# Kernel tuning notes

Hardware: AMD Instinct MI355X
Metric: run time of the kernel (lower is better)

## Reference

```python
import jax, jax.numpy as jnp
import numpy as np

NUM_INPUTS = 16
NUM_HIDDEN = 256
NUM_LAYERS = 4
B = 16384


def setup_inputs() -> dict:
    key = jax.random.key(0)
    ks = jax.random.split(key, 8)
    H, N, L = NUM_HIDDEN, NUM_INPUTS, NUM_LAYERS
    x0 = jax.random.normal(ks[0], (B, N), dtype=jnp.float32)
    # input layer: Linear(2 -> H)
    W_in = jax.random.normal(ks[1], (2, H), dtype=jnp.float32) * (1.0 / np.sqrt(2.0))
    b_in = jnp.zeros((H,), dtype=jnp.float32)
    # L-1 intermediate layers: Linear(2H -> H), stacked
    W_mid = jax.random.normal(ks[2], (L - 1, 2 * H, H), dtype=jnp.float32) * (1.0 / np.sqrt(2.0 * H))
    b_mid = jnp.zeros((L - 1, H), dtype=jnp.float32)
    # slater: Linear(H -> N) with xavier-normal weight, zero bias
    W_sl = jax.random.normal(ks[3], (H, N), dtype=jnp.float32) * np.sqrt(2.0 / (H + N))
    b_sl = jnp.zeros((N,), dtype=jnp.float32)
    width = jnp.full((1,), 0.1, dtype=jnp.float32)
    return {"x0": x0, "W_in": W_in, "b_in": b_in, "W_mid": W_mid,
            "b_mid": b_mid, "W_sl": W_sl, "b_sl": b_sl, "width": width}


def _forward(x0, W_in, b_in, W_mid, b_mid, W_sl, b_sl, width):
    N = x0.shape[1]
    # input equivariant layer: f = stack(h, mean(h)) -> [B, N, 2]
    g = jnp.broadcast_to(x0.mean(axis=1, keepdims=True), x0.shape)
    f = jnp.stack((x0, g), axis=2)                       # [B, N, 2]
    h = jnp.tanh(jnp.einsum('bnf,fh->bnh', f, W_in) + b_in)  # [B, N, H]
    # intermediate equivariant layers with residual
    for i in range(W_mid.shape[0]):
        gm = jnp.broadcast_to(h.mean(axis=1, keepdims=True), h.shape)
        fm = jnp.concatenate((h, gm), axis=2)            # [B, N, 2H]
        h = jnp.tanh(jnp.einsum('bnf,fh->bnh', fm, W_mid[i]) + b_mid[i]) + h
    # slog slater determinant
    slater = jnp.einsum('bnh,hm->bnm', h, W_sl) + b_sl   # [B, N, N]
    sign, logabsdet = jnp.linalg.slogdet(slater)
    log_factorial = jnp.log(jnp.arange(1, N + 1, dtype=jnp.float32)).sum()
    log_bcs = -width[0] * jnp.sum(x0 ** 2, axis=1)       # [B]
    return sign, logabsdet - 0.5 * log_factorial + log_bcs


def reference(x0, W_in, b_in, W_mid, b_mid, W_sl, b_sl, width):
    return _forward(x0, W_in, b_in, W_mid, b_mid, W_sl, b_sl, width)
```

## Files before the change

kernel.cpp:

```cpp
#include <hip/hip_runtime.h>

#define BTOT 16384
#define NI   16
#define HD   256
#define BB   4
#define NMID 3
#define ASH  264
#define SLS  20
#define HALF_LOGFACT 15.3359295387f

typedef short  bf16x8 __attribute__((ext_vector_type(8)));
typedef float  f32x4  __attribute__((ext_vector_type(4)));

__device__ __forceinline__ unsigned short f2bf(float f) {
    unsigned u = __builtin_bit_cast(unsigned, f);
    u += 0x7FFFu + ((u >> 16) & 1u);
    return (unsigned short)(u >> 16);
}
__device__ __forceinline__ unsigned cvt_pk_bf16(float lo, float hi) {
    unsigned d;
    asm("v_cvt_pk_bf16_f32 %0, %1, %2" : "=v"(d) : "v"(lo), "v"(hi));
    return d;
}
__device__ __forceinline__ float bflo(unsigned u) { return __builtin_bit_cast(float, u << 16); }
__device__ __forceinline__ float bfhi(unsigned u) { return __builtin_bit_cast(float, u & 0xFFFF0000u); }
__device__ __forceinline__ float bcast(float x, int lane) {
    return __builtin_bit_cast(float,
        __builtin_amdgcn_readlane(__builtin_bit_cast(int, x), lane));
}
__device__ __forceinline__ float tanh5(float x) {
    float z = __builtin_amdgcn_exp2f(x * 2.885390081777927f);
    return __builtin_fmaf(-2.0f, __builtin_amdgcn_rcpf(1.0f + z), 1.0f);
}
#define LGKM_BAR() do { asm volatile("s_waitcnt lgkmcnt(0)" ::: "memory"); \
    __builtin_amdgcn_s_barrier(); __builtin_amdgcn_sched_barrier(0); } while (0)
#define LGKM_WAIT() do { asm volatile("s_waitcnt lgkmcnt(0)" ::: "memory"); \
    __builtin_amdgcn_sched_barrier(0); } while (0)

__global__ void prep_w(const float* __restrict__ Wmid, const float* __restrict__ Wsl,
                       unsigned short* __restrict__ wtc) {
    const int b = blockIdx.x;
    const int t = threadIdx.x;
    unsigned short* dst = wtc + (size_t)b * 8192;
    if (b < 48) {
        const int layer = b >> 4, ch = b & 15;
        const float* src = Wmid + (size_t)layer * (2 * HD * HD);
#pragma unroll 4
        for (int v = 0; v < 32; ++v) {
            int o = t * 32 + v;
            int kk = o & 7, j = (o >> 3) & 15, kg = o >> 7;
            dst[o] = f2bf(src[(8 * kg + kk) * HD + ch * 16 + j]);
        }
    } else {
#pragma unroll 4
        for (int v = 0; v < 32; ++v) {
            int o = t * 32 + v;
            int kk = o & 7, j = (o >> 3) & 15, kg = o >> 7;
            dst[o] = (kg < 32) ? f2bf(Wsl[(8 * kg + kk) * NI + j]) : (unsigned short)0;
        }
    }
}

struct __align__(16) SMem {
    union {
        unsigned short h[BB * NI * ASH];
        float slf[BB][NI * ASH / 2];
    } u;
    unsigned short gm[BB * HD];
};
static_assert(sizeof(SMem) == 35840, "LDS fine");

__global__ __launch_bounds__(256, 2)
void eqslater_mfma(const float* __restrict__ x0g,
                   const float* __restrict__ Win,
                   const float* __restrict__ bin,
                   const float* __restrict__ bmid,
                   const float* __restrict__ bsl,
                   const float* __restrict__ width,
                   const unsigned short* __restrict__ wtc,
                   float* __restrict__ out) {
    __shared__ SMem sm;
    const int tid = threadIdx.x;
    const int bbase = blockIdx.x * BB;
    const int w = tid >> 6;
    const int l = tid & 63;
    const int c = l & 15;
    const int g = l >> 4;
    const int j4 = 4 * g;
    const int B0 = 64 * w;

    const unsigned short* wlane = wtc + (size_t)g * 128 + (size_t)c * 8;

    float x0v = x0g[bbase * NI + l];
    {
        float ssum = x0v;
#pragma unroll
        for (int off = 8; off > 0; off >>= 1) ssum += __shfl_xor(ssum, off);
        x0v = x0v;
        const float gme = ssum * 0.0625f;
        const int jc = B0 + l;
        const float w0 = Win[jc], w1 = Win[HD + jc], bj = bin[jc];
#pragma unroll
        for (int el = 0; el < 4; ++el) {
            float ge = bcast(gme, el * 16);
            float gl = __builtin_fmaf(ge, w1, bj);
#pragma unroll 4
            for (int r = 0; r < NI; ++r) {
                float xv = bcast(x0v, el * 16 + r);
                float f = tanh5(__builtin_fmaf(xv, w0, gl));
                sm.u.h[(el * NI + r) * ASH + jc] =
                    (unsigned short)cvt_pk_bf16(f, f);
            }
        }
    }
    LGKM_BAR();

    bf16x8 afE[4][8], agm[8], wf[8];

#pragma unroll 1
    for (int layer = 0; layer < NMID; ++layer) {
#pragma unroll
        for (int el = 0; el < 4; ++el)
#pragma unroll
            for (int s = 0; s < 8; ++s)
                afE[el][s] = *(const bf16x8*)&sm.u.h[(el * NI + c) * ASH + 32 * s + 8 * g];
        {
            const int el2 = l >> 4;
            const int c0 = B0 + (l & 15) * 4;
            float s0 = 0, s1 = 0, s2 = 0, s3 = 0;
#pragma unroll
            for (int r = 0; r < NI; ++r) {
                uint2 d = *(const uint2*)&sm.u.h[(el2 * NI + r) * ASH + c0];
                s0 += bflo(d.x); s1 += bfhi(d.x);
                s2 += bflo(d.y); s3 += bfhi(d.y);
            }
            uint2 go;
            go.x = cvt_pk_bf16(s0 * 0.0625f, s1 * 0.0625f);
            go.y = cvt_pk_bf16(s2 * 0.0625f, s3 * 0.0625f);
            *(uint2*)&sm.gm[el2 * HD + c0] = go;
        }
        LGKM_BAR();
#pragma unroll
        for (int s = 0; s < 8; ++s)
            agm[s] = *(const bf16x8*)&sm.gm[(c & 3) * HD + 32 * s + 8 * g];

        const float* bml = bmid + layer * HD;

#pragma unroll 1
        for (int cc = 0; cc < 4; ++cc) {
            const int ch = 4 * w + cc;
            const int fc = layer * 16 + ch;
            const unsigned short* cb = wlane + (size_t)fc * 8192;

#pragma unroll
            for (int s = 0; s < 8; ++s)
                wf[s] = *(const bf16x8*)(cb + 4096 + s * 512);
            f32x4 accG = {0.f, 0.f, 0.f, 0.f};
#pragma unroll
            for (int s = 0; s < 8; ++s)
                accG = __builtin_amdgcn_mfma_f32_16x16x32_bf16(wf[s], agm[s], accG, 0, 0, 0);
            const float4 bv = *(const float4*)&bml[ch * 16 + j4];
            accG[0] += bv.x; accG[1] += bv.y; accG[2] += bv.z; accG[3] += bv.w;

#pragma unroll
            for (int s = 0; s < 8; ++s)
                wf[s] = *(const bf16x8*)(cb + s * 512);

#pragma unroll
            for (int el = 0; el < 4; ++el) {
                const int src = (l & 48) + el;
                float gv0 = __shfl(accG[0], src);
                float gv1 = __shfl(accG[1], src);
                float gv2 = __shfl(accG[2], src);
                float gv3 = __shfl(accG[3], src);
                f32x4 acc = {0.f, 0.f, 0.f, 0.f};
#pragma unroll
                for (int s = 0; s < 8; ++s)
                    acc = __builtin_amdgcn_mfma_f32_16x16x32_bf16(wf[s], afE[el][s], acc, 0, 0, 0);
                unsigned short* hrow = &sm.u.h[(el * NI + c) * ASH + ch * 16 + j4];
                uint2 hd2 = *(const uint2*)hrow;
                float f0 = tanh5(acc[0] + gv0) + bflo(hd2.x);
                float f1 = tanh5(acc[1] + gv1) + bfhi(hd2.x);
                float f2 = tanh5(acc[2] + gv2) + bflo(hd2.y);
                float f3 = tanh5(acc[3] + gv3) + bfhi(hd2.y);
                uint2 wo; wo.x = cvt_pk_bf16(f0, f1); wo.y = cvt_pk_bf16(f2, f3);
                *(uint2*)hrow = wo;
            }
        }
        LGKM_BAR();
    }

    {
        const int e = w;
        bf16x8 afs[8];
#pragma unroll
        for (int s = 0; s < 8; ++s)
            afs[s] = *(const bf16x8*)&sm.u.h[(e * NI + c) * ASH + 32 * s + 8 * g];
        const unsigned short* cb = wlane + (size_t)48 * 8192;
        f32x4 a0 = {0.f,0.f,0.f,0.f}, a1 = {0.f,0.f,0.f,0.f};
#pragma unroll
        for (int s = 0; s < 4; ++s) {
            bf16x8 b0 = *(const bf16x8*)(cb + (2 * s) * 512);
            bf16x8 b1 = *(const bf16x8*)(cb + (2 * s + 1) * 512);
            a0 = __builtin_amdgcn_mfma_f32_16x16x32_bf16(b0, afs[2 * s],     a0, 0, 0, 0);
            a1 = __builtin_amdgcn_mfma_f32_16x16x32_bf16(b1, afs[2 * s + 1], a1, 0, 0, 0);
        }
        f32x4 sv = a0 + a1;
        const float4 bsv = *(const float4*)&bsl[j4];
        float* slp = &sm.u.slf[e][0];
        float4 o;
        o.x = sv[0] + bsv.x; o.y = sv[1] + bsv.y;
        o.z = sv[2] + bsv.z; o.w = sv[3] + bsv.w;
        *(float4*)&slp[c * SLS + j4] = o;
    }
    LGKM_WAIT();

    {
        const int e = w;
        const float* slp = &sm.u.slf[e][0];
        const int i = c;
        float M[16];
#pragma unroll
        for (int jj = 0; jj < 4; ++jj) {
            float4 vv = *(const float4*)&slp[i * SLS + 4 * jj];
            M[4 * jj] = vv.x; M[4 * jj + 1] = vv.y; M[4 * jj + 2] = vv.z; M[4 * jj + 3] = vv.w;
        }

        int elim = 0;
        unsigned chosen = 0;
        int invcnt = 0;
        float dsign = 1.f, logabs = 0.f;
#pragma unroll
        for (int k = 0; k < 16; ++k) {
            float myv = elim ? -1.f : __builtin_fabsf(M[k]);
            float maxv = myv;
#pragma unroll
            for (int off = 8; off > 0; off >>= 1)
                maxv = fmaxf(maxv, __shfl_xor(maxv, off));
            unsigned long long bal = __ballot(myv == maxv);
            const int p = (__ffsll((long long)bal) - 1) & 15;

            invcnt += __popc(chosen >> (p + 1));
            chosen |= 1u << p;
            if (i == p) elim = 1;

            float piv = bcast(M[k], p);
            float ap = fmaxf(__builtin_fabsf(piv), 1e-35f);
            logabs += __logf(ap);
            if (piv < 0.f) dsign = -dsign;
            float spiv = __builtin_copysignf(ap, piv);
            float mi = __fdividef(M[k], spiv);
#pragma unroll
            for (int j = k + 1; j < 16; ++j) {
                float pr = bcast(M[j], p);
                if (!elim) M[j] = __builtin_fmaf(-mi, pr, M[j]);
            }
        }
        if (invcnt & 1) dsign = -dsign;

        float xv = (l < NI) ? x0g[(bbase + w) * NI + l] : 0.f;
        float sq = xv * xv;
#pragma unroll
        for (int off = 8; off > 0; off >>= 1) sq += __shfl_xor(sq, off);

        if (l == 0) {
            out[bbase + w] = dsign;
            out[BTOT + bbase + w] = logabs - HALF_LOGFACT - width[0] * sq;
        }
    }
}

extern "C" void kernel_launch(void* const* d_in, const int* in_sizes, int n_in,
                              void* d_out, int out_size, void* d_ws, size_t ws_size,
                              hipStream_t stream) {
    const float* x0   = (const float*)d_in[0];
    const float* Win  = (const float*)d_in[1];
    const float* bin  = (const float*)d_in[2];
    const float* Wmid = (const float*)d_in[3];
    const float* bmid = (const float*)d_in[4];
    const float* Wsl  = (const float*)d_in[5];
    const float* bsl  = (const float*)d_in[6];
    const float* wid  = (const float*)d_in[7];
    float* out = (float*)d_out;

    unsigned short* wtc = (unsigned short*)d_ws;

    hipLaunchKernelGGL(prep_w, dim3(49), dim3(256), 0, stream, Wmid, Wsl, wtc);
    hipLaunchKernelGGL(eqslater_mfma, dim3(BTOT / BB), dim3(256), 0, stream,
                       x0, Win, bin, bmid, bsl, wid, wtc, out);
}
```

Before: 273.7 us.

## Cut register pressure by stashing half the activations in LDS for 3 blocks/CU

Register-resident A fragments are halved: only the first two batch elements stay in VGPRs, while the other two are copied into a new LDS stash region at the start of each layer and reloaded per output chunk. The global-mean fragments are also reloaded from LDS per chunk instead of held in registers. Launch bounds rise from 2 to 3 blocks per CU to raise occupancy and hide latency. The trade-off is extra LDS traffic for the stash copy and the repeated fragment reloads, plus a larger LDS footprint per block.

```diff
diff --git a/kernel.cpp b/kernel.cpp
--- a/kernel.cpp
+++ b/kernel.cpp
@@ -66,11 +66,12 @@
         unsigned short h[BB * NI * ASH];
         float slf[BB][NI * ASH / 2];
     } u;
+    unsigned short stash[2 * NI * ASH];
     unsigned short gm[BB * HD];
 };
-static_assert(sizeof(SMem) == 35840, "LDS fine");
-
-__global__ __launch_bounds__(256, 2)
+static_assert(sizeof(SMem) == 52736, "R6-proven 3-blocks/CU size");
+
+__global__ __launch_bounds__(256, 3)
 void eqslater_mfma(const float* __restrict__ x0g,
                    const float* __restrict__ Win,
                    const float* __restrict__ bin,
@@ -96,7 +97,6 @@
         float ssum = x0v;
 #pragma unroll
         for (int off = 8; off > 0; off >>= 1) ssum += __shfl_xor(ssum, off);
-        x0v = x0v;
         const float gme = ssum * 0.0625f;
         const int jc = B0 + l;
         const float w0 = Win[jc], w1 = Win[HD + jc], bj = bin[jc];
@@ -115,15 +115,24 @@
     }
     LGKM_BAR();
 
-    bf16x8 afE[4][8], agm[8], wf[8];
+    bf16x8 afE[2][8], wf[8], sbuf[8];
 
 #pragma unroll 1
     for (int layer = 0; layer < NMID; ++layer) {
 #pragma unroll
-        for (int el = 0; el < 4; ++el)
+        for (int el = 0; el < 2; ++el)
 #pragma unroll
             for (int s = 0; s < 8; ++s)
                 afE[el][s] = *(const bf16x8*)&sm.u.h[(el * NI + c) * ASH + 32 * s + 8 * g];
+        {
+            const int r32 = tid >> 3;
+            const int seg = tid & 7;
+            const unsigned short* srcp = &sm.u.h[(32 + r32) * ASH + seg * 32];
+            unsigned short* dstp = &sm.stash[r32 * ASH + seg * 32];
+#pragma unroll
+            for (int p = 0; p < 4; ++p)
+                *(uint4*)(dstp + p * 8) = *(const uint4*)(srcp + p * 8);
+        }
         {
             const int el2 = l >> 4;
             const int c0 = B0 + (l & 15) * 4;
@@ -140,9 +149,6 @@
             *(uint2*)&sm.gm[el2 * HD + c0] = go;
         }
         LGKM_BAR();
-#pragma unroll
-        for (int s = 0; s < 8; ++s)
-            agm[s] = *(const bf16x8*)&sm.gm[(c & 3) * HD + 32 * s + 8 * g];
 
         const float* bml = bmid + layer * HD;
 
@@ -153,12 +159,14 @@
             const unsigned short* cb = wlane + (size_t)fc * 8192;
 
 #pragma unroll
+            for (int s = 0; s < 8; ++s) {
+                wf[s]   = *(const bf16x8*)(cb + 4096 + s * 512);
+                sbuf[s] = *(const bf16x8*)&sm.gm[(c & 3) * HD + 32 * s + 8 * g];
+            }
+            f32x4 accG = {0.f, 0.f, 0.f, 0.f};
+#pragma unroll
             for (int s = 0; s < 8; ++s)
-                wf[s] = *(const bf16x8*)(cb + 4096 + s * 512);
-            f32x4 accG = {0.f, 0.f, 0.f, 0.f};
-#pragma unroll
-            for (int s = 0; s < 8; ++s)
-                accG = __builtin_amdgcn_mfma_f32_16x16x32_bf16(wf[s], agm[s], accG, 0, 0, 0);
+                accG = __builtin_amdgcn_mfma_f32_16x16x32_bf16(wf[s], sbuf[s], accG, 0, 0, 0);
             const float4 bv = *(const float4*)&bml[ch * 16 + j4];
             accG[0] += bv.x; accG[1] += bv.y; accG[2] += bv.z; accG[3] += bv.w;
 
@@ -167,7 +175,7 @@
                 wf[s] = *(const bf16x8*)(cb + s * 512);
 
 #pragma unroll
-            for (int el = 0; el < 4; ++el) {
+            for (int el = 0; el < 2; ++el) {
                 const int src = (l & 48) + el;
                 float gv0 = __shfl(accG[0], src);
                 float gv1 = __shfl(accG[1], src);
@@ -186,24 +194,46 @@
                 uint2 wo; wo.x = cvt_pk_bf16(f0, f1); wo.y = cvt_pk_bf16(f2, f3);
                 *(uint2*)hrow = wo;
             }
+#pragma unroll
+            for (int el = 2; el < 4; ++el) {
+#pragma unroll
+                for (int s = 0; s < 8; ++s)
+                    sbuf[s] = *(const bf16x8*)&sm.stash[((el - 2) * NI + c) * ASH + 32 * s + 8 * g];
+                const int src = (l & 48) + el;
+                float gv0 = __shfl(accG[0], src);
+                float gv1 = __shfl(accG[1], src);
+                float gv2 = __shfl(accG[2], src);
+                float gv3 = __shfl(accG[3], src);
+                f32x4 acc = {0.f, 0.f, 0.f, 0.f};
+#pragma unroll
+                for (int s = 0; s < 8; ++s)
+                    acc = __builtin_amdgcn_mfma_f32_16x16x32_bf16(wf[s], sbuf[s], acc, 0, 0, 0);
+                unsigned short* hrow = &sm.u.h[(el * NI + c) * ASH + ch * 16 + j4];
+                uint2 hd2 = *(const uint2*)hrow;
+                float f0 = tanh5(acc[0] + gv0) + bflo(hd2.x);
+                float f1 = tanh5(acc[1] + gv1) + bfhi(hd2.x);
+                float f2 = tanh5(acc[2] + gv2) + bflo(hd2.y);
+                float f3 = tanh5(acc[3] + gv3) + bfhi(hd2.y);
+                uint2 wo; wo.x = cvt_pk_bf16(f0, f1); wo.y = cvt_pk_bf16(f2, f3);
+                *(uint2*)hrow = wo;
+            }
         }
         LGKM_BAR();
     }
 
     {
         const int e = w;
-        bf16x8 afs[8];
 #pragma unroll
         for (int s = 0; s < 8; ++s)
-            afs[s] = *(const bf16x8*)&sm.u.h[(e * NI + c) * ASH + 32 * s + 8 * g];
+            sbuf[s] = *(const bf16x8*)&sm.u.h[(e * NI + c) * ASH + 32 * s + 8 * g];
         const unsigned short* cb = wlane + (size_t)48 * 8192;
         f32x4 a0 = {0.f,0.f,0.f,0.f}, a1 = {0.f,0.f,0.f,0.f};
 #pragma unroll
         for (int s = 0; s < 4; ++s) {
             bf16x8 b0 = *(const bf16x8*)(cb + (2 * s) * 512);
             bf16x8 b1 = *(const bf16x8*)(cb + (2 * s + 1) * 512);
-            a0 = __builtin_amdgcn_mfma_f32_16x16x32_bf16(b0, afs[2 * s],     a0, 0, 0, 0);
-            a1 = __builtin_amdgcn_mfma_f32_16x16x32_bf16(b1, afs[2 * s + 1], a1, 0, 0, 0);
+            a0 = __builtin_amdgcn_mfma_f32_16x16x32_bf16(b0, sbuf[2 * s],     a0, 0, 0, 0);
+            a1 = __builtin_amdgcn_mfma_f32_16x16x32_bf16(b1, sbuf[2 * s + 1], a1, 0, 0, 0);
         }
         f32x4 sv = a0 + a1;
         const float4 bsv = *(const float4*)&bsl[j4];
```

Result: faster. 257.8 us (-5.8%).
